# Kernel tuning notes

Measured on AMD Instinct MI355X. Metric: run time of the kernel, lower is better.

The kernel has to match this reference:

```python
import jax, jax.numpy as jnp
import numpy as np

L = 2
NB = (L + 1) ** 2      # 9 spherical-harmonic basis components
C = 256                # in_channels == out_channels
MID = C // 4           # 64, mid_channels in the FF
N = 4096               # nodes
K = 16                 # neighbors (neighbor_cg)


def _real_sh_l2(rel):
    # Real spherical harmonics up to l=2 of normalized edge directions. rel: [N,K,3] -> [N,K,9]
    r = jnp.sqrt(jnp.sum(rel * rel, axis=-1, keepdims=True))
    d = rel / (r + 1e-8)
    x, y, z = d[..., 0], d[..., 1], d[..., 2]
    c0 = 0.28209479177387814
    c1 = 0.4886025119029199
    c2 = 1.0925484305920792
    c2b = 0.31539156525252005
    c2c = 0.5462742152960396
    return jnp.stack([
        jnp.full_like(x, c0),
        c1 * y, c1 * z, c1 * x,
        c2 * x * y, c2 * y * z, c2b * (3.0 * z * z - 1.0), c2 * x * z, c2c * (x * x - y * y),
    ], axis=-1)


def setup_inputs() -> dict:
    key = jax.random.key(0)
    ks = jax.random.split(key, 8)
    return {
        "s_feats": jax.random.normal(ks[0], (N, NB, C), jnp.float32),
        "s_points": jax.random.normal(ks[1], (N, 3), jnp.float32),
        "cg": jax.random.normal(ks[2], (NB, NB, NB), jnp.float32) * 0.1,  # CG coefficient buffer
        "W_proj": jax.random.normal(ks[3], (C, C), jnp.float32) / np.sqrt(C),
        "ln_w": jnp.ones((L + 1, C), jnp.float32),
        "ln_b": jnp.zeros((C,), jnp.float32),
        "W_ff1": jax.random.normal(ks[4], (C, MID), jnp.float32) / np.sqrt(C),
        "W_gate": jax.random.normal(ks[5], (MID, MID * (L + 1)), jnp.float32) / np.sqrt(MID),
        "W_ff2": jax.random.normal(ks[6], (MID, C), jnp.float32) / np.sqrt(MID),
        "neighbor_indices": jax.random.randint(ks[7], (N, K), 0, N),
    }


def _forward(s_feats, s_points, cg, W_proj, ln_w, ln_b, W_ff1, W_gate, W_ff2, neighbor_indices):
    # --- CGConv: project, gather neighbors, SH of edge directions, CG tensor product, mean-aggregate ---
    h = jnp.einsum('nic,co->nio', s_feats, W_proj)               # [N,9,C]
    nbr = h[neighbor_indices]                                    # [N,K,9,C] irregular gather
    rel = s_points[neighbor_indices] - s_points[:, None, :]      # [N,K,3]
    sh = _real_sh_l2(rel)                                        # [N,K,9]
    x = jnp.einsum('nkic,nkj,ijo->noc', nbr, sh, cg) / K         # [N,9,C]
    # --- residual add of input (linear3 == Identity since in_channels == out_channels) ---
    x = x + s_feats
    shortcut = x
    # --- EquivariantLayerNormV2: per-degree RMS norm; mean-center + bias only on l=0 ---
    outs = []
    for l in range(L + 1):
        f = x[:, l * l:(l + 1) * (l + 1), :]                     # [N,2l+1,C]
        if l == 0:
            f = f - jnp.mean(f, axis=-1, keepdims=True)
        nrm = jnp.mean(f * f, axis=(1, 2), keepdims=True)
        f = f * jax.lax.rsqrt(nrm + 1e-5) * ln_w[l][None, None, :]
        if l == 0:
            f = f + ln_b[None, None, :]
        outs.append(f)
    y = jnp.concatenate(outs, axis=1)
    # --- FF: Linear -> Gate_3j -> Linear, residual ---
    z = jnp.einsum('nic,cm->nim', y, W_ff1)                      # [N,9,MID]
    after = z[:, 0, :] @ W_gate                                  # [N, MID*(L+1)]
    t0 = jax.nn.silu(after[:, :MID])
    mult = jax.nn.sigmoid(after[:, MID:])                        # [N, MID*L]
    gated = [t0[:, None, :]]
    for l in range(1, L + 1):
        gated.append(z[:, l * l:(l + 1) * (l + 1), :] * mult[:, None, (l - 1) * MID:l * MID])
    z = jnp.concatenate(gated, axis=1)                           # [N,9,MID]
    return jnp.einsum('nim,mc->nic', z, W_ff2) + shortcut


def reference(s_feats, s_points, cg, W_proj, ln_w, ln_b, W_ff1, W_gate, W_ff2, neighbor_indices):
    return _forward(s_feats, s_points, cg, W_proj, ln_w, ln_b, W_ff1, W_gate, W_ff2, neighbor_indices)
```

## Files before the change

kernel.cpp:

```cpp
#include <hip/hip_runtime.h>
#include <hip/hip_bf16.h>

#define N_PTS  4096
#define NB     9
#define C      256
#define MID    64
#define KNBR   16
#define NROWS  (N_PTS * NB)

typedef __attribute__((ext_vector_type(8))) short     short8;
typedef __attribute__((ext_vector_type(4))) float     f32x4;
typedef __attribute__((ext_vector_type(2))) float     f32x2;
typedef __attribute__((ext_vector_type(4))) unsigned short ush4;

static __device__ __forceinline__ unsigned short f2bf(float f) {
    union { float f; unsigned u; } v; v.f = f;
    unsigned u = v.u + 0x7FFFu + ((v.u >> 16) & 1u);
    return (unsigned short)(u >> 16);
}
static __device__ __forceinline__ float bf2f(unsigned short s) {
    union { unsigned u; float f; } v; v.u = ((unsigned)s) << 16;
    return v.f;
}

#if __has_builtin(__builtin_elementwise_fma)
static __device__ __forceinline__ f32x2 fma2(f32x2 a, f32x2 b, f32x2 c) {
    return __builtin_elementwise_fma(a, b, c);
}
#else
static __device__ __forceinline__ f32x2 fma2(f32x2 a, f32x2 b, f32x2 c) {
    f32x2 r; r.x = fmaf(a.x, b.x, c.x); r.y = fmaf(a.y, b.y, c.y); return r;
}
#endif

#define LDK 40
__global__ __launch_bounds__(256) void k_proj(const float* __restrict__ A,
                                              const float* __restrict__ W,
                                              unsigned short* __restrict__ H) {
    __shared__ unsigned short As[128 * LDK];
    __shared__ unsigned short Bs[128 * LDK];
    const int tid = threadIdx.x;
    const int r0  = blockIdx.x * 128;
    const int n0  = blockIdx.y * 128;
    const int wave = tid >> 6, lane = tid & 63;
    const int wm = wave >> 1, wn = wave & 1;
    const int lr = lane & 15, lg = lane >> 4;

    f32x4 acc[4][4];
#pragma unroll
    for (int a = 0; a < 4; ++a)
#pragma unroll
        for (int b = 0; b < 4; ++b) acc[a][b] = (f32x4){0.f, 0.f, 0.f, 0.f};

    for (int k0 = 0; k0 < C; k0 += 32) {
        __syncthreads();
#pragma unroll
        for (int rep = 0; rep < 4; ++rep) {
            const int e   = rep * 256 + tid;
            const int row = e >> 3;
            const int c4  = (e & 7) << 2;
            const float4 v = *reinterpret_cast<const float4*>(&A[(size_t)(r0 + row) * C + k0 + c4]);
            ush4 s = { f2bf(v.x), f2bf(v.y), f2bf(v.z), f2bf(v.w) };
            *reinterpret_cast<ush4*>(&As[row * LDK + c4]) = s;
        }
#pragma unroll
        for (int rep = 0; rep < 4; ++rep) {
            const int e = rep * 256 + tid;
            const int k = e >> 5;
            const int j = (e & 31) << 2;
            const float4 v = *reinterpret_cast<const float4*>(&W[(size_t)(k0 + k) * C + n0 + j]);
            Bs[(j + 0) * LDK + k] = f2bf(v.x);
            Bs[(j + 1) * LDK + k] = f2bf(v.y);
            Bs[(j + 2) * LDK + k] = f2bf(v.z);
            Bs[(j + 3) * LDK + k] = f2bf(v.w);
        }
        __syncthreads();

        short8 af[4], bfr[4];
#pragma unroll
        for (int mf = 0; mf < 4; ++mf)
            af[mf] = *reinterpret_cast<const short8*>(&As[(wm * 64 + mf * 16 + lr) * LDK + lg * 8]);
#pragma unroll
        for (int nf = 0; nf < 4; ++nf)
            bfr[nf] = *reinterpret_cast<const short8*>(&Bs[(wn * 64 + nf * 16 + lr) * LDK + lg * 8]);
#pragma unroll
        for (int mf = 0; mf < 4; ++mf)
#pragma unroll
            for (int nf = 0; nf < 4; ++nf)
                acc[mf][nf] = __builtin_amdgcn_mfma_f32_16x16x32_bf16(af[mf], bfr[nf], acc[mf][nf], 0, 0, 0);
    }
#pragma unroll
    for (int mf = 0; mf < 4; ++mf)
#pragma unroll
        for (int nf = 0; nf < 4; ++nf) {
            const int col = n0 + wn * 64 + nf * 16 + lr;
#pragma unroll
            for (int r = 0; r < 4; ++r) {
                const int row = r0 + wm * 64 + mf * 16 + lg * 4 + r;
                H[(size_t)row * C + col] = f2bf(acc[mf][nf][r]);
            }
        }
}

__global__ __launch_bounds__(128) void k_cg_ln(const unsigned short* __restrict__ Hb,
                                               const float* __restrict__ s_feats,
                                               const float* __restrict__ pts,
                                               const float* __restrict__ cg,
                                               const int*   __restrict__ nbr,
                                               const float* __restrict__ ln_w,
                                               const float* __restrict__ ln_b,
                                               unsigned short* __restrict__ Xb,
                                               unsigned short* __restrict__ Yb) {
    __shared__ float cg_s[729];
    __shared__ float sh_s[2][KNBR][NB];
    __shared__ float w_s[2][KNBR * 81];
    __shared__ int   idx_s[2][KNBR];

    const int tid  = threadIdx.x;
    const int wid  = tid >> 6;
    const int lane = tid & 63;
    const int n    = blockIdx.x * 2 + wid;

    for (int e = tid; e < 729; e += 128) cg_s[e] = cg[e];

    if (lane < KNBR) {
        const int idx = nbr[n * KNBR + lane];
        idx_s[wid][lane] = idx;
        const float px = pts[idx * 3 + 0] - pts[n * 3 + 0];
        const float py = pts[idx * 3 + 1] - pts[n * 3 + 1];
        const float pz = pts[idx * 3 + 2] - pts[n * 3 + 2];
        const float r  = sqrtf(px * px + py * py + pz * pz);
        const float iv = 1.f / (r + 1e-8f);
        const float dx = px * iv, dy = py * iv, dz = pz * iv;
        const float c1 = 0.4886025119029199f;
        const float c2 = 1.0925484305920792f;
        sh_s[wid][lane][0] = 0.28209479177387814f;
        sh_s[wid][lane][1] = c1 * dy;
        sh_s[wid][lane][2] = c1 * dz;
        sh_s[wid][lane][3] = c1 * dx;
        sh_s[wid][lane][4] = c2 * dx * dy;
        sh_s[wid][lane][5] = c2 * dy * dz;
        sh_s[wid][lane][6] = 0.31539156525252005f * (3.f * dz * dz - 1.f);
        sh_s[wid][lane][7] = c2 * dx * dz;
        sh_s[wid][lane][8] = 0.5462742152960396f * (dx * dx - dy * dy);
    }
    __syncthreads();

    for (int t = lane; t < KNBR * 81; t += 64) {
        const int k   = t / 81;
        const int rem = t - k * 81;
        const int i   = rem / 9;
        const int o   = rem - i * 9;
        float s = 0.f;
#pragma unroll
        for (int j = 0; j < 9; ++j) s = fmaf(sh_s[wid][k][j], cg_s[i * 81 + j * 9 + o], s);
        w_s[wid][t] = s;
    }
    __syncthreads();

    const int c0 = lane * 4;
    f32x2 acc[9][2];
#pragma unroll
    for (int o = 0; o < 9; ++o) { acc[o][0] = (f32x2){0.f, 0.f}; acc[o][1] = (f32x2){0.f, 0.f}; }

    for (int k = 0; k < KNBR; ++k) {
        const unsigned short* hrow = Hb + (size_t)idx_s[wid][k] * (NB * C) + c0;
        const float* wk = &w_s[wid][k * 81];
#pragma unroll
        for (int i = 0; i < 9; ++i) {
            const ush4 q = *reinterpret_cast<const ush4*>(hrow + (size_t)i * C);
            const f32x2 h01 = { bf2f(q.x), bf2f(q.y) };
            const f32x2 h23 = { bf2f(q.z), bf2f(q.w) };
#pragma unroll
            for (int o = 0; o < 9; ++o) {
                const float w = wk[i * 9 + o];
                const f32x2 wv = { w, w };
                acc[o][0] = fma2(h01, wv, acc[o][0]);
                acc[o][1] = fma2(h23, wv, acc[o][1]);
            }
        }
    }

    const float* sf = s_feats + (size_t)n * (NB * C) + c0;
    f32x2 v[9][2];
#pragma unroll
    for (int o = 0; o < 9; ++o) {
        const float4 s4 = *reinterpret_cast<const float4*>(sf + (size_t)o * C);
        v[o][0].x = acc[o][0].x * (1.f / (float)KNBR) + s4.x;
        v[o][0].y = acc[o][0].y * (1.f / (float)KNBR) + s4.y;
        v[o][1].x = acc[o][1].x * (1.f / (float)KNBR) + s4.z;
        v[o][1].y = acc[o][1].y * (1.f / (float)KNBR) + s4.w;
    }

    float s0 = v[0][0].x + v[0][0].y + v[0][1].x + v[0][1].y;
    float s1 = v[0][0].x * v[0][0].x + v[0][0].y * v[0][0].y +
               v[0][1].x * v[0][1].x + v[0][1].y * v[0][1].y;
    float s2 = 0.f, s3 = 0.f;
#pragma unroll
    for (int o = 1; o < 4; ++o)
        s2 += v[o][0].x * v[o][0].x + v[o][0].y * v[o][0].y +
              v[o][1].x * v[o][1].x + v[o][1].y * v[o][1].y;
#pragma unroll
    for (int o = 4; o < 9; ++o)
        s3 += v[o][0].x * v[o][0].x + v[o][0].y * v[o][0].y +
              v[o][1].x * v[o][1].x + v[o][1].y * v[o][1].y;
#pragma unroll
    for (int off = 32; off >= 1; off >>= 1) {
        s0 += __shfl_xor(s0, off);
        s1 += __shfl_xor(s1, off);
        s2 += __shfl_xor(s2, off);
        s3 += __shfl_xor(s3, off);
    }

    const float mean0 = s0 * (1.f / 256.f);
    const float nrm0  = s1 * (1.f / 256.f) - mean0 * mean0;
    const float nrm1  = s2 * (1.f / 768.f);
    const float nrm2  = s3 * (1.f / 1280.f);
    const float r0 = rsqrtf(nrm0 + 1e-5f);
    const float r1 = rsqrtf(nrm1 + 1e-5f);
    const float r2 = rsqrtf(nrm2 + 1e-5f);

    const float4 lw0 = *reinterpret_cast<const float4*>(ln_w + c0);
    const float4 lw1 = *reinterpret_cast<const float4*>(ln_w + C + c0);
    const float4 lw2 = *reinterpret_cast<const float4*>(ln_w + 2 * C + c0);
    const float4 lb0 = *reinterpret_cast<const float4*>(ln_b + c0);

    unsigned short* xo = Xb + (size_t)n * (NB * C) + c0;
    unsigned short* yo = Yb + (size_t)n * (NB * C) + c0;
#pragma unroll
    for (int o = 0; o < 9; ++o) {
        ush4 s = { f2bf(v[o][0].x), f2bf(v[o][0].y), f2bf(v[o][1].x), f2bf(v[o][1].y) };
        *reinterpret_cast<ush4*>(xo + (size_t)o * C) = s;
    }
    {
        ush4 s = { f2bf((v[0][0].x - mean0) * r0 * lw0.x + lb0.x),
                   f2bf((v[0][0].y - mean0) * r0 * lw0.y + lb0.y),
                   f2bf((v[0][1].x - mean0) * r0 * lw0.z + lb0.z),
                   f2bf((v[0][1].y - mean0) * r0 * lw0.w + lb0.w) };
        *reinterpret_cast<ush4*>(yo) = s;
    }
#pragma unroll
    for (int o = 1; o < 4; ++o) {
        ush4 s = { f2bf(v[o][0].x * r1 * lw1.x), f2bf(v[o][0].y * r1 * lw1.y),
                   f2bf(v[o][1].x * r1 * lw1.z), f2bf(v[o][1].y * r1 * lw1.w) };
        *reinterpret_cast<ush4*>(yo + (size_t)o * C) = s;
    }
#pragma unroll
    for (int o = 4; o < 9; ++o) {
        ush4 s = { f2bf(v[o][0].x * r2 * lw2.x), f2bf(v[o][0].y * r2 * lw2.y),
                   f2bf(v[o][1].x * r2 * lw2.z), f2bf(v[o][1].y * r2 * lw2.w) };
        *reinterpret_cast<ush4*>(yo + (size_t)o * C) = s;
    }
}

__global__ __launch_bounds__(256) void k_ff1(const unsigned short* __restrict__ Yb,
                                             const float* __restrict__ W1,
                                             unsigned short* __restrict__ Zb) {
    __shared__ unsigned short As[128 * LDK];
    __shared__ unsigned short Bs[64 * LDK];
    const int tid = threadIdx.x;
    const int r0  = blockIdx.x * 128;
    const int wave = tid >> 6, lane = tid & 63;
    const int wm = wave >> 1, wn = wave & 1;
    const int lr = lane & 15, lg = lane >> 4;

    f32x4 acc[4][2];
#pragma unroll
    for (int a = 0; a < 4; ++a) { acc[a][0] = (f32x4){0.f,0.f,0.f,0.f}; acc[a][1] = (f32x4){0.f,0.f,0.f,0.f}; }

    for (int k0 = 0; k0 < C; k0 += 32) {
        __syncthreads();
#pragma unroll
        for (int rep = 0; rep < 4; ++rep) {
            const int e   = rep * 256 + tid;
            const int row = e >> 3;
            const int c4  = (e & 7) << 2;
            ush4 s = *reinterpret_cast<const ush4*>(&Yb[(size_t)(r0 + row) * C + k0 + c4]);
            *reinterpret_cast<ush4*>(&As[row * LDK + c4]) = s;
        }
#pragma unroll
        for (int rep = 0; rep < 2; ++rep) {
            const int e = rep * 256 + tid;
            const int k = e >> 4;
            const int j = (e & 15) << 2;
            const float4 v = *reinterpret_cast<const float4*>(&W1[(size_t)(k0 + k) * MID + j]);
            Bs[(j + 0) * LDK + k] = f2bf(v.x);
            Bs[(j + 1) * LDK + k] = f2bf(v.y);
            Bs[(j + 2) * LDK + k] = f2bf(v.z);
            Bs[(j + 3) * LDK + k] = f2bf(v.w);
        }
        __syncthreads();

        short8 af[4], bfr[2];
#pragma unroll
        for (int mf = 0; mf < 4; ++mf)
            af[mf] = *reinterpret_cast<const short8*>(&As[(wm * 64 + mf * 16 + lr) * LDK + lg * 8]);
#pragma unroll
        for (int nf = 0; nf < 2; ++nf)
            bfr[nf] = *reinterpret_cast<const short8*>(&Bs[(wn * 32 + nf * 16 + lr) * LDK + lg * 8]);
#pragma unroll
        for (int mf = 0; mf < 4; ++mf)
#pragma unroll
            for (int nf = 0; nf < 2; ++nf)
                acc[mf][nf] = __builtin_amdgcn_mfma_f32_16x16x32_bf16(af[mf], bfr[nf], acc[mf][nf], 0, 0, 0);
    }
#pragma unroll
    for (int mf = 0; mf < 4; ++mf)
#pragma unroll
        for (int nf = 0; nf < 2; ++nf) {
            const int col = wn * 32 + nf * 16 + lr;
#pragma unroll
            for (int r = 0; r < 4; ++r) {
                const int row = r0 + wm * 64 + mf * 16 + lg * 4 + r;
                Zb[(size_t)row * MID + col] = f2bf(acc[mf][nf][r]);
            }
        }
}

__global__ __launch_bounds__(192) void k_gate(const unsigned short* __restrict__ Zb,
                                              const float* __restrict__ Wg,
                                              float* __restrict__ G) {
    __shared__ float wgs[64 * 192];
    __shared__ float z0s[16 * 64];
    const int tid = threadIdx.x;
    const int n0  = blockIdx.x * 16;

    for (int e = tid; e < 64 * 192; e += 192) wgs[e] = Wg[e];
    for (int e = tid; e < 16 * 64; e += 192) {
        const int r = e >> 6, m = e & 63;
        z0s[e] = bf2f(Zb[(size_t)(n0 + r) * (NB * MID) + m]);
    }
    __syncthreads();

    const int j = tid;
    for (int r = 0; r < 16; ++r) {
        float acc = 0.f;
        for (int m0 = 0; m0 < 64; m0 += 4) {
            const float4 zv = *reinterpret_cast<const float4*>(&z0s[r * 64 + m0]);
            acc = fmaf(zv.x, wgs[(m0 + 0) * 192 + j], acc);
            acc = fmaf(zv.y, wgs[(m0 + 1) * 192 + j], acc);
            acc = fmaf(zv.z, wgs[(m0 + 2) * 192 + j], acc);
            acc = fmaf(zv.w, wgs[(m0 + 3) * 192 + j], acc);
        }
        const float sig = 1.f / (1.f + expf(-acc));
        G[(size_t)(n0 + r) * 192 + j] = (j < 64) ? acc * sig : sig;
    }
}

#define LDK64 72
__global__ __launch_bounds__(256) void k_final(const unsigned short* __restrict__ Zb,
                                               const float* __restrict__ G,
                                               const float* __restrict__ W2,
                                               const unsigned short* __restrict__ Xb,
                                               float* __restrict__ OUT) {
    __shared__ unsigned short As[128 * LDK64];
    __shared__ unsigned short Bs[128 * LDK64];
    const int tid = threadIdx.x;
    const int r0  = blockIdx.x * 128;
    const int n0  = blockIdx.y * 128;
    const int wave = tid >> 6, lane = tid & 63;
    const int wm = wave >> 1, wn = wave & 1;
    const int lr = lane & 15, lg = lane >> 4;

    {
        const int arow = tid >> 1;
        const int kh   = (tid & 1) * 32;
        const int grow = r0 + arow;
        const int nn   = grow / 9;
        const int ii   = grow - nn * 9;
        if (ii == 0) {
            const float* gp = &G[(size_t)nn * 192 + kh];
#pragma unroll
            for (int j = 0; j < 32; j += 4) {
                const float4 g = *reinterpret_cast<const float4*>(&gp[j]);
                ush4 s = { f2bf(g.x), f2bf(g.y), f2bf(g.z), f2bf(g.w) };
                *reinterpret_cast<ush4*>(&As[arow * LDK64 + kh + j]) = s;
            }
        } else {
            const float* gm = &G[(size_t)nn * 192 + ((ii < 4) ? 64 : 128) + kh];
            const unsigned short* zr = &Zb[(size_t)nn * (NB * MID) + ii * MID + kh];
#pragma unroll
            for (int j = 0; j < 32; j += 4) {
                const ush4 zv = *reinterpret_cast<const ush4*>(&zr[j]);
                const float4 g = *reinterpret_cast<const float4*>(&gm[j]);
                ush4 s = { f2bf(bf2f(zv.x) * g.x), f2bf(bf2f(zv.y) * g.y),
                           f2bf(bf2f(zv.z) * g.z), f2bf(bf2f(zv.w) * g.w) };
                *reinterpret_cast<ush4*>(&As[arow * LDK64 + kh + j]) = s;
            }
        }
    }
#pragma unroll
    for (int rep = 0; rep < 8; ++rep) {
        const int e = rep * 256 + tid;
        const int k = e >> 5;
        const int j = (e & 31) << 2;
        const float4 v = *reinterpret_cast<const float4*>(&W2[(size_t)k * C + n0 + j]);
        Bs[(j + 0) * LDK64 + k] = f2bf(v.x);
        Bs[(j + 1) * LDK64 + k] = f2bf(v.y);
        Bs[(j + 2) * LDK64 + k] = f2bf(v.z);
        Bs[(j + 3) * LDK64 + k] = f2bf(v.w);
    }
    __syncthreads();

    f32x4 acc[4][4];
#pragma unroll
    for (int a = 0; a < 4; ++a)
#pragma unroll
        for (int b = 0; b < 4; ++b) acc[a][b] = (f32x4){0.f, 0.f, 0.f, 0.f};

#pragma unroll
    for (int ks = 0; ks < 2; ++ks) {
        short8 af[4], bfr[4];
#pragma unroll
        for (int mf = 0; mf < 4; ++mf)
            af[mf] = *reinterpret_cast<const short8*>(&As[(wm * 64 + mf * 16 + lr) * LDK64 + ks * 32 + lg * 8]);
#pragma unroll
        for (int nf = 0; nf < 4; ++nf)
            bfr[nf] = *reinterpret_cast<const short8*>(&Bs[(wn * 64 + nf * 16 + lr) * LDK64 + ks * 32 + lg * 8]);
#pragma unroll
        for (int mf = 0; mf < 4; ++mf)
#pragma unroll
            for (int nf = 0; nf < 4; ++nf)
                acc[mf][nf] = __builtin_amdgcn_mfma_f32_16x16x32_bf16(af[mf], bfr[nf], acc[mf][nf], 0, 0, 0);
    }

#pragma unroll
    for (int mf = 0; mf < 4; ++mf)
#pragma unroll
        for (int nf = 0; nf < 4; ++nf) {
            const int col = n0 + wn * 64 + nf * 16 + lr;
#pragma unroll
            for (int r = 0; r < 4; ++r) {
                const int row = r0 + wm * 64 + mf * 16 + lg * 4 + r;
                OUT[(size_t)row * C + col] = acc[mf][nf][r] + bf2f(Xb[(size_t)row * C + col]);
            }
        }
}

extern "C" void kernel_launch(void* const* d_in, const int* in_sizes, int n_in,
                              void* d_out, int out_size, void* d_ws, size_t ws_size,
                              hipStream_t stream) {
    const float* s_feats = (const float*)d_in[0];
    const float* s_pts   = (const float*)d_in[1];
    const float* cg      = (const float*)d_in[2];
    const float* W_proj  = (const float*)d_in[3];
    const float* ln_w    = (const float*)d_in[4];
    const float* ln_b    = (const float*)d_in[5];
    const float* W_ff1   = (const float*)d_in[6];
    const float* W_gate  = (const float*)d_in[7];
    const float* W_ff2   = (const float*)d_in[8];
    const int*   nbr     = (const int*)d_in[9];
    float* out = (float*)d_out;

    unsigned short* Hb = (unsigned short*)d_ws;
    unsigned short* Xb = Hb + (size_t)NROWS * C;
    unsigned short* Yb = Xb + (size_t)NROWS * C;
    unsigned short* Zb = Yb + (size_t)NROWS * C;
    float* G = (float*)(Zb + (size_t)NROWS * MID);

    k_proj  <<<dim3(NROWS / 128, 2), 256, 0, stream>>>(s_feats, W_proj, Hb);
    k_cg_ln <<<N_PTS / 2,            128, 0, stream>>>(Hb, s_feats, s_pts, cg, nbr, ln_w, ln_b, Xb, Yb);
    k_ff1   <<<NROWS / 128,          256, 0, stream>>>(Yb, W_ff1, Zb);
    k_gate  <<<N_PTS / 16,           192, 0, stream>>>(Zb, W_gate, G);
    k_final <<<dim3(NROWS / 128, 2), 256, 0, stream>>>(Zb, G, W_ff2, Xb, out);
}
```

Before: 127.8 us.

## Split CG-conv channels across two waves per node to double parallelism

```diff
diff --git a/kernel.cpp b/kernel.cpp
--- a/kernel.cpp
+++ b/kernel.cpp
@@ -14,13 +14,22 @@
 typedef __attribute__((ext_vector_type(4))) unsigned short ush4;
 
 static __device__ __forceinline__ unsigned short f2bf(float f) {
-    union { float f; unsigned u; } v; v.f = f;
-    unsigned u = v.u + 0x7FFFu + ((v.u >> 16) & 1u);
-    return (unsigned short)(u >> 16);
+    union { __hip_bfloat16 h; unsigned short u; } cv;
+    cv.h = __float2bfloat16(f);
+    return cv.u;
 }
 static __device__ __forceinline__ float bf2f(unsigned short s) {
     union { unsigned u; float f; } v; v.u = ((unsigned)s) << 16;
     return v.f;
+}
+static __device__ __forceinline__ f32x2 bf2x2(unsigned u) {
+    union { unsigned u; float f; } lo, hi;
+    lo.u = u << 16;
+    hi.u = u & 0xffff0000u;
+    return (f32x2){lo.f, hi.f};
+}
+static __device__ __forceinline__ unsigned packbf(float a, float b) {
+    return (unsigned)f2bf(a) | ((unsigned)f2bf(b) << 16);
 }
 
 #if __has_builtin(__builtin_elementwise_fma)
@@ -102,7 +111,7 @@
         }
 }
 
-__global__ __launch_bounds__(128) void k_cg_ln(const unsigned short* __restrict__ Hb,
+__global__ __launch_bounds__(256) void k_cg_ln(const unsigned short* __restrict__ Hb,
                                                const float* __restrict__ s_feats,
                                                const float* __restrict__ pts,
                                                const float* __restrict__ cg,
@@ -115,95 +124,93 @@
     __shared__ float sh_s[2][KNBR][NB];
     __shared__ float w_s[2][KNBR * 81];
     __shared__ int   idx_s[2][KNBR];
+    __shared__ float red_s[2][2][4];
 
     const int tid  = threadIdx.x;
-    const int wid  = tid >> 6;
+    const int wave = tid >> 6;
     const int lane = tid & 63;
-    const int n    = blockIdx.x * 2 + wid;
-
-    for (int e = tid; e < 729; e += 128) cg_s[e] = cg[e];
-
-    if (lane < KNBR) {
-        const int idx = nbr[n * KNBR + lane];
-        idx_s[wid][lane] = idx;
-        const float px = pts[idx * 3 + 0] - pts[n * 3 + 0];
-        const float py = pts[idx * 3 + 1] - pts[n * 3 + 1];
-        const float pz = pts[idx * 3 + 2] - pts[n * 3 + 2];
+    const int p    = wave >> 1;
+    const int half = wave & 1;
+    const int n    = blockIdx.x * 2 + p;
+    const int ch   = half * 128 + lane * 2;
+
+    for (int e = tid; e < 729; e += 256) cg_s[e] = cg[e];
+
+    if (tid < 2 * KNBR) {
+        const int pp = tid >> 4, kk = tid & 15;
+        const int nn = blockIdx.x * 2 + pp;
+        const int idx = nbr[nn * KNBR + kk];
+        idx_s[pp][kk] = idx;
+        const float px = pts[idx * 3 + 0] - pts[nn * 3 + 0];
+        const float py = pts[idx * 3 + 1] - pts[nn * 3 + 1];
+        const float pz = pts[idx * 3 + 2] - pts[nn * 3 + 2];
         const float r  = sqrtf(px * px + py * py + pz * pz);
         const float iv = 1.f / (r + 1e-8f);
         const float dx = px * iv, dy = py * iv, dz = pz * iv;
         const float c1 = 0.4886025119029199f;
         const float c2 = 1.0925484305920792f;
-        sh_s[wid][lane][0] = 0.28209479177387814f;
-        sh_s[wid][lane][1] = c1 * dy;
-        sh_s[wid][lane][2] = c1 * dz;
-        sh_s[wid][lane][3] = c1 * dx;
-        sh_s[wid][lane][4] = c2 * dx * dy;
-        sh_s[wid][lane][5] = c2 * dy * dz;
-        sh_s[wid][lane][6] = 0.31539156525252005f * (3.f * dz * dz - 1.f);
-        sh_s[wid][lane][7] = c2 * dx * dz;
-        sh_s[wid][lane][8] = 0.5462742152960396f * (dx * dx - dy * dy);
+        sh_s[pp][kk][0] = 0.28209479177387814f;
+        sh_s[pp][kk][1] = c1 * dy;
+        sh_s[pp][kk][2] = c1 * dz;
+        sh_s[pp][kk][3] = c1 * dx;
+        sh_s[pp][kk][4] = c2 * dx * dy;
+        sh_s[pp][kk][5] = c2 * dy * dz;
+        sh_s[pp][kk][6] = 0.31539156525252005f * (3.f * dz * dz - 1.f);
+        sh_s[pp][kk][7] = c2 * dx * dz;
+        sh_s[pp][kk][8] = 0.5462742152960396f * (dx * dx - dy * dy);
     }
     __syncthreads();
 
-    for (int t = lane; t < KNBR * 81; t += 64) {
+    for (int t = half * 64 + lane; t < KNBR * 81; t += 128) {
         const int k   = t / 81;
         const int rem = t - k * 81;
         const int i   = rem / 9;
         const int o   = rem - i * 9;
         float s = 0.f;
 #pragma unroll
-        for (int j = 0; j < 9; ++j) s = fmaf(sh_s[wid][k][j], cg_s[i * 81 + j * 9 + o], s);
-        w_s[wid][t] = s;
+        for (int j = 0; j < 9; ++j) s = fmaf(sh_s[p][k][j], cg_s[i * 81 + j * 9 + o], s);
+        w_s[p][t] = s;
     }
     __syncthreads();
 
-    const int c0 = lane * 4;
-    f32x2 acc[9][2];
-#pragma unroll
-    for (int o = 0; o < 9; ++o) { acc[o][0] = (f32x2){0.f, 0.f}; acc[o][1] = (f32x2){0.f, 0.f}; }
+    f32x2 acc[9];
+#pragma unroll
+    for (int o = 0; o < 9; ++o) acc[o] = (f32x2){0.f, 0.f};
 
     for (int k = 0; k < KNBR; ++k) {
-        const unsigned short* hrow = Hb + (size_t)idx_s[wid][k] * (NB * C) + c0;
-        const float* wk = &w_s[wid][k * 81];
+        const unsigned* hrow =
+            reinterpret_cast<const unsigned*>(Hb + (size_t)idx_s[p][k] * (NB * C) + ch);
+        unsigned q[9];
+#pragma unroll
+        for (int i = 0; i < 9; ++i) q[i] = hrow[i * (C / 2)];
+        const float* wk = &w_s[p][k * 81];
 #pragma unroll
         for (int i = 0; i < 9; ++i) {
-            const ush4 q = *reinterpret_cast<const ush4*>(hrow + (size_t)i * C);
-            const f32x2 h01 = { bf2f(q.x), bf2f(q.y) };
-            const f32x2 h23 = { bf2f(q.z), bf2f(q.w) };
+            const f32x2 h = bf2x2(q[i]);
 #pragma unroll
             for (int o = 0; o < 9; ++o) {
                 const float w = wk[i * 9 + o];
-                const f32x2 wv = { w, w };
-                acc[o][0] = fma2(h01, wv, acc[o][0]);
-                acc[o][1] = fma2(h23, wv, acc[o][1]);
-            }
-        }
-    }
-
-    const float* sf = s_feats + (size_t)n * (NB * C) + c0;
-    f32x2 v[9][2];
+                acc[o] = fma2(h, (f32x2){w, w}, acc[o]);
+            }
+        }
+    }
+
+    const float2* sf = reinterpret_cast<const float2*>(s_feats + (size_t)n * (NB * C) + ch);
+    f32x2 v[9];
 #pragma unroll
     for (int o = 0; o < 9; ++o) {
-        const float4 s4 = *reinterpret_cast<const float4*>(sf + (size_t)o * C);
-        v[o][0].x = acc[o][0].x * (1.f / (float)KNBR) + s4.x;
-        v[o][0].y = acc[o][0].y * (1.f / (float)KNBR) + s4.y;
-        v[o][1].x = acc[o][1].x * (1.f / (float)KNBR) + s4.z;
-        v[o][1].y = acc[o][1].y * (1.f / (float)KNBR) + s4.w;
-    }
-
-    float s0 = v[0][0].x + v[0][0].y + v[0][1].x + v[0][1].y;
-    float s1 = v[0][0].x * v[0][0].x + v[0][0].y * v[0][0].y +
-               v[0][1].x * v[0][1].x + v[0][1].y * v[0][1].y;
+        const float2 s2 = sf[o * (C / 2)];
+        v[o].x = acc[o].x * (1.f / (float)KNBR) + s2.x;
+        v[o].y = acc[o].y * (1.f / (float)KNBR) + s2.y;
+    }
+
+    float s0 = v[0].x + v[0].y;
+    float s1 = v[0].x * v[0].x + v[0].y * v[0].y;
     float s2 = 0.f, s3 = 0.f;
 #pragma unroll
-    for (int o = 1; o < 4; ++o)
-        s2 += v[o][0].x * v[o][0].x + v[o][0].y * v[o][0].y +
-              v[o][1].x * v[o][1].x + v[o][1].y * v[o][1].y;
-#pragma unroll
-    for (int o = 4; o < 9; ++o)
-        s3 += v[o][0].x * v[o][0].x + v[o][0].y * v[o][0].y +
-              v[o][1].x * v[o][1].x + v[o][1].y * v[o][1].y;
+    for (int o = 1; o < 4; ++o) s2 += v[o].x * v[o].x + v[o].y * v[o].y;
+#pragma unroll
+    for (int o = 4; o < 9; ++o) s3 += v[o].x * v[o].x + v[o].y * v[o].y;
 #pragma unroll
     for (int off = 32; off >= 1; off >>= 1) {
         s0 += __shfl_xor(s0, off);
@@ -211,6 +218,15 @@
         s2 += __shfl_xor(s2, off);
         s3 += __shfl_xor(s3, off);
     }
+    if (lane == 0) {
+        red_s[p][half][0] = s0; red_s[p][half][1] = s1;
+        red_s[p][half][2] = s2; red_s[p][half][3] = s3;
+    }
+    __syncthreads();
+    s0 = red_s[p][0][0] + red_s[p][1][0];
+    s1 = red_s[p][0][1] + red_s[p][1][1];
+    s2 = red_s[p][0][2] + red_s[p][1][2];
+    s3 = red_s[p][0][3] + red_s[p][1][3];
 
     const float mean0 = s0 * (1.f / 256.f);
     const float nrm0  = s1 * (1.f / 256.f) - mean0 * mean0;
@@ -220,37 +236,23 @@
     const float r1 = rsqrtf(nrm1 + 1e-5f);
     const float r2 = rsqrtf(nrm2 + 1e-5f);
 
-    const float4 lw0 = *reinterpret_cast<const float4*>(ln_w + c0);
-    const float4 lw1 = *reinterpret_cast<const float4*>(ln_w + C + c0);
-    const float4 lw2 = *reinterpret_cast<const float4*>(ln_w + 2 * C + c0);
-    const float4 lb0 = *reinterpret_cast<const float4*>(ln_b + c0);
-
-    unsigned short* xo = Xb + (size_t)n * (NB * C) + c0;
-    unsigned short* yo = Yb + (size_t)n * (NB * C) + c0;
-#pragma unroll
-    for (int o = 0; o < 9; ++o) {
-        ush4 s = { f2bf(v[o][0].x), f2bf(v[o][0].y), f2bf(v[o][1].x), f2bf(v[o][1].y) };
-        *reinterpret_cast<ush4*>(xo + (size_t)o * C) = s;
-    }
-    {
-        ush4 s = { f2bf((v[0][0].x - mean0) * r0 * lw0.x + lb0.x),
-                   f2bf((v[0][0].y - mean0) * r0 * lw0.y + lb0.y),
-                   f2bf((v[0][1].x - mean0) * r0 * lw0.z + lb0.z),
-                   f2bf((v[0][1].y - mean0) * r0 * lw0.w + lb0.w) };
-        *reinterpret_cast<ush4*>(yo) = s;
-    }
-#pragma unroll
-    for (int o = 1; o < 4; ++o) {
-        ush4 s = { f2bf(v[o][0].x * r1 * lw1.x), f2bf(v[o][0].y * r1 * lw1.y),
-                   f2bf(v[o][1].x * r1 * lw1.z), f2bf(v[o][1].y * r1 * lw1.w) };
-        *reinterpret_cast<ush4*>(yo + (size_t)o * C) = s;
-    }
-#pragma unroll
-    for (int o = 4; o < 9; ++o) {
-        ush4 s = { f2bf(v[o][0].x * r2 * lw2.x), f2bf(v[o][0].y * r2 * lw2.y),
-                   f2bf(v[o][1].x * r2 * lw2.z), f2bf(v[o][1].y * r2 * lw2.w) };
-        *reinterpret_cast<ush4*>(yo + (size_t)o * C) = s;
-    }
+    const float2 lw0 = *reinterpret_cast<const float2*>(ln_w + ch);
+    const float2 lw1 = *reinterpret_cast<const float2*>(ln_w + C + ch);
+    const float2 lw2 = *reinterpret_cast<const float2*>(ln_w + 2 * C + ch);
+    const float2 lb0 = *reinterpret_cast<const float2*>(ln_b + ch);
+
+    unsigned* xo = reinterpret_cast<unsigned*>(Xb + (size_t)n * (NB * C) + ch);
+    unsigned* yo = reinterpret_cast<unsigned*>(Yb + (size_t)n * (NB * C) + ch);
+#pragma unroll
+    for (int o = 0; o < 9; ++o) xo[o * (C / 2)] = packbf(v[o].x, v[o].y);
+    yo[0] = packbf((v[0].x - mean0) * r0 * lw0.x + lb0.x,
+                   (v[0].y - mean0) * r0 * lw0.y + lb0.y);
+#pragma unroll
+    for (int o = 1; o < 4; ++o)
+        yo[o * (C / 2)] = packbf(v[o].x * r1 * lw1.x, v[o].y * r1 * lw1.y);
+#pragma unroll
+    for (int o = 4; o < 9; ++o)
+        yo[o * (C / 2)] = packbf(v[o].x * r2 * lw2.x, v[o].y * r2 * lw2.y);
 }
 
 __global__ __launch_bounds__(256) void k_ff1(const unsigned short* __restrict__ Yb,
@@ -459,7 +461,7 @@
     float* G = (float*)(Zb + (size_t)NROWS * MID);
 
     k_proj  <<<dim3(NROWS / 128, 2), 256, 0, stream>>>(s_feats, W_proj, Hb);
-    k_cg_ln <<<N_PTS / 2,            128, 0, stream>>>(Hb, s_feats, s_pts, cg, nbr, ln_w, ln_b, Xb, Yb);
+    k_cg_ln <<<N_PTS / 2,            256, 0, stream>>>(Hb, s_feats, s_pts, cg, nbr, ln_w, ln_b, Xb, Yb);
     k_ff1   <<<NROWS / 128,          256, 0, stream>>>(Yb, W_ff1, Zb);
     k_gate  <<<N_PTS / 16,           192, 0, stream>>>(Zb, W_gate, G);
     k_final <<<dim3(NROWS / 128, 2), 256, 0, stream>>>(Zb, G, W_ff2, Xb, out);
```

Measured after the change: 133.7 us. 4.7% more time.
